# Optimization experiments

Measured on AMD Instinct MI355X. Metric: run time of the kernel, lower is better.

The kernel has to match this reference:

```python
import jax, jax.numpy as jnp
import numpy as np

N, E, C, D, M = 20000, 640000, 128, 128, 128


def setup_inputs() -> dict:
    key = jax.random.key(0)
    ks = jax.random.split(key, 16)
    g = lambda k, shape, fan: jax.random.normal(k, shape, jnp.float32) * (1.0 / np.sqrt(fan))
    return {
        "x": jax.random.normal(ks[0], (N, C), jnp.float32),
        "edge_index": jax.random.randint(ks[1], (2, E), 0, N, jnp.int64),
        "W_src": g(ks[2], (C, D), C),
        "b_src": jnp.zeros((D,), jnp.float32),
        "W_tgt": g(ks[3], (C, D), C),
        "W_skip": g(ks[4], (C, D), C),
        "a0": jnp.asarray(0.2, jnp.float32),   # PReLU init=0.2
        "W1": g(ks[5], (D, M), D),
        "b1": jnp.zeros((M,), jnp.float32),
        "a1": jnp.asarray(0.25, jnp.float32),  # MLP PReLU default
        "W2": g(ks[6], (M, D), M),
        "b2": jnp.zeros((D,), jnp.float32),
        "Wg": g(ks[7], (D, 1), D),
        "gamma": jnp.ones((D,), jnp.float32),
        "beta": jnp.zeros((D,), jnp.float32),
    }


def _prelu(h, a):
    return jnp.where(h >= 0, h, a * h)


def reference(x, edge_index, W_src, b_src, W_tgt, W_skip, a0, W1, b1, a1, W2, b2, Wg, gamma, beta):
    n = x.shape[0]
    j, i = edge_index[0], edge_index[1]  # src -> tgt
    msg_src = x @ W_src + b_src          # lin_src (bias)
    msg_tgt = x @ W_tgt                  # lin_tgt (no bias)
    # per-edge message: msg_nn(msg_j + msg_i) = PReLU -> Linear -> PReLU -> Linear
    h = _prelu(msg_src[j] + msg_tgt[i], a0)          # [E, D]
    h = _prelu(h @ W1 + b1, a1)                      # [E, M]
    msg = h @ W2 + b2                                # [E, D]
    # gate + sparse softmax over edges grouped by target node i
    gate = msg @ Wg                                  # [E, 1]
    gmax = jax.ops.segment_max(gate, i, num_segments=n)
    eg = jnp.exp(gate - gmax[i])
    gsum = jax.ops.segment_sum(eg, i, num_segments=n)
    alpha = eg / (gsum[i] + 1e-16)                   # [E, 1]
    # aggregate (aggr='add')
    out = jax.ops.segment_sum(alpha * msg, i, num_segments=n)  # [N, D]
    # root/skip connection
    out = out + x @ W_skip
    # LayerNorm
    mu = jnp.mean(out, axis=-1, keepdims=True)
    var = jnp.var(out, axis=-1, keepdims=True)
    out = (out - mu) * jax.lax.rsqrt(var + 1e-5) * gamma + beta
    return out
```

## Files before the change

### kernel.cpp

```cpp
#include <hip/hip_runtime.h>
#include <hip/hip_bf16.h>
#include <stdint.h>

#define DIM 128
#define HSTR 136
#define H2STR 72
#define NPB 16
#define NMAX 20224

using hfrag = __attribute__((ext_vector_type(8))) _Float16;
using h2v   = __attribute__((ext_vector_type(2))) _Float16;
using f32x4 = __attribute__((ext_vector_type(4))) float;

__device__ __forceinline__ float prelu_f(float v, float a) { return v >= 0.f ? v : a * v; }

__device__ __forceinline__ unsigned pkh(float a, float b) {
    auto h = __builtin_amdgcn_cvt_pkrtz(a, b);
    return *(unsigned*)&h;
}
__device__ __forceinline__ unsigned short hs(float v) {
    _Float16 h = (_Float16)v;
    return *(unsigned short*)&h;
}
__device__ __forceinline__ unsigned prelu2_add(unsigned su, unsigned gu, h2v a2) {
    h2v s = *(h2v*)&su, g = *(h2v*)&gu;
    h2v h = s + g;
    h2v z = {(_Float16)0.f, (_Float16)0.f};
    h2v mx = __builtin_elementwise_max(h, z);
    h2v mn = __builtin_elementwise_min(h, z);
    h2v r = mn * a2 + mx;
    return *(unsigned*)&r;
}

__global__ __launch_bounds__(256) void prep_hist_k(
    const float* __restrict__ Wsrc, const float* __restrict__ Wtgt,
    const float* __restrict__ Wskip, const float* __restrict__ W1,
    const float* __restrict__ W2, const float* __restrict__ b2,
    const float* __restrict__ Wg,
    unsigned short* __restrict__ Wall, float* __restrict__ w2g,
    const int* __restrict__ eidx, int E, int* __restrict__ deg,
    int* __restrict__ rank)
{
    const int nhist = (E + 255) / 256;
    if ((int)blockIdx.x < nhist) {
        const int e = blockIdx.x * 256 + threadIdx.x;
        if (e < E) rank[e] = atomicAdd(deg + eidx[(size_t)E + e], 1);
        return;
    }
    const int b = blockIdx.x - nhist;
    if (b == (5 * DIM * DIM) / 256) {
        const int k = threadIdx.x;
        if (k < DIM) {
            float s = 0.f;
            for (int d = 0; d < DIM; ++d) s += W2[k * DIM + d] * Wg[d];
            w2g[k] = s;
        } else if (k == DIM) {
            float s = 0.f;
            for (int d = 0; d < DIM; ++d) s += b2[d] * Wg[d];
            w2g[DIM] = s;
        }
        return;
    }
    const int idx = b * 256 + threadIdx.x;
    const int m = idx >> 14;
    const int r = idx & 16383;
    const int n = r >> 7, k = r & 127;
    const float* W = (m == 0) ? Wsrc : (m == 1) ? Wtgt : (m == 2) ? Wskip : (m == 3) ? W1 : W2;
    const _Float16 hv = (_Float16)W[k * DIM + n];
    Wall[idx] = *(const unsigned short*)&hv;
}

__global__ __launch_bounds__(1024) void scan_k(const int* __restrict__ deg,
                                               int* __restrict__ rowptr, int N)
{
    __shared__ int part[1024];
    const int t = threadIdx.x;

    if (N <= NMAX) {
        __shared__ int s[NMAX];
        for (int k = t; k < N; k += 1024) s[k] = deg[k];
        __syncthreads();

        const int chunk = (N + 1023) / 1024;
        const int lo = min(t * chunk, N), hi = min(lo + chunk, N);
        int sum = 0;
        for (int k = lo; k < hi; ++k) sum += s[k];
        part[t] = sum;
        __syncthreads();
        for (int off = 1; off < 1024; off <<= 1) {
            int u = (t >= off) ? part[t - off] : 0;
            __syncthreads();
            part[t] += u;
            __syncthreads();
        }
        int run = part[t] - sum;
        for (int k = lo; k < hi; ++k) { const int d = s[k]; s[k] = run; run += d; }
        __syncthreads();
        for (int k = t; k < N; k += 1024) rowptr[k] = s[k];
        if (t == 0) rowptr[N] = part[1023];
    } else {
        const int chunk = (N + 1023) / 1024;
        const int lo = min(t * chunk, N), hi = min(lo + chunk, N);
        int s = 0;
        for (int k = lo; k < hi; ++k) s += deg[k];
        part[t] = s;
        __syncthreads();
        for (int off = 1; off < 1024; off <<= 1) {
            int u = (t >= off) ? part[t - off] : 0;
            __syncthreads();
            part[t] += u;
            __syncthreads();
        }
        int run = part[t] - s;
        for (int k = lo; k < hi; ++k) {
            rowptr[k] = run;
            run += deg[k];
        }
        if (t == 1023) rowptr[N] = part[1023];
    }
}

__global__ __launch_bounds__(256) void scatter_node_k(
    const int* __restrict__ eidx, int E,
    const int* __restrict__ rowptr, const int* __restrict__ rank,
    int2* __restrict__ jip, int nscatter,
    const float* __restrict__ x,
    const unsigned short* __restrict__ Wall,
    const float* __restrict__ bsrc,
    unsigned short* __restrict__ msg_src, unsigned short* __restrict__ msg_tgt,
    float* __restrict__ skip, int N)
{
    if ((int)blockIdx.x < nscatter) {
        const int e = blockIdx.x * 256 + threadIdx.x;
        if (e < E) {
            const int j = eidx[e];
            const int i = eidx[(size_t)E + e];
            const int p = rowptr[i] + rank[e];
            jip[p] = make_int2(j, i);
        }
        return;
    }

    __shared__ unsigned short xt[32 * HSTR];
    const int t = threadIdx.x;
    const int n0blk = (blockIdx.x - nscatter) * 32;
    const int w = t >> 6, lane = t & 63, col = lane & 15, quad = lane >> 4;

    for (int k = t; k < 32 * 16; k += 256) {
        const int row = k >> 4, o = k & 15;
        uint4 v = make_uint4(0, 0, 0, 0);
        if (n0blk + row < N) {
            const float4 a = *(const float4*)(x + (size_t)(n0blk + row) * DIM + o * 8);
            const float4 b = *(const float4*)(x + (size_t)(n0blk + row) * DIM + o * 8 + 4);
            v.x = pkh(a.x, a.y); v.y = pkh(a.z, a.w);
            v.z = pkh(b.x, b.y); v.w = pkh(b.z, b.w);
        }
        *(uint4*)(xt + row * HSTR + o * 8) = v;
    }
    __syncthreads();

    hfrag af[2][4];
    #pragma unroll
    for (int mt = 0; mt < 2; ++mt)
        #pragma unroll
        for (int ks = 0; ks < 4; ++ks)
            af[mt][ks] = *(const hfrag*)(xt + (mt * 16 + col) * HSTR + ks * 32 + quad * 8);

    for (int m = 0; m < 3; ++m) {
        const unsigned short* Wt = Wall + m * DIM * DIM;
        hfrag bw[2][4];
        #pragma unroll
        for (int nt = 0; nt < 2; ++nt)
            #pragma unroll
            for (int ks = 0; ks < 4; ++ks)
                bw[nt][ks] = *(const hfrag*)(Wt + (w * 32 + nt * 16 + col) * DIM + ks * 32 + quad * 8);

        f32x4 acc[2][2];
        #pragma unroll
        for (int mt = 0; mt < 2; ++mt)
            #pragma unroll
            for (int nt = 0; nt < 2; ++nt)
                acc[mt][nt] = f32x4{0.f, 0.f, 0.f, 0.f};

        #pragma unroll
        for (int mt = 0; mt < 2; ++mt)
            #pragma unroll
            for (int nt = 0; nt < 2; ++nt)
                #pragma unroll
                for (int ks = 0; ks < 4; ++ks)
                    acc[mt][nt] = __builtin_amdgcn_mfma_f32_16x16x32_f16(
                        bw[nt][ks], af[mt][ks], acc[mt][nt], 0, 0, 0);

        #pragma unroll
        for (int mt = 0; mt < 2; ++mt) {
            const int node = n0blk + mt * 16 + col;
            if (node >= N) continue;
            #pragma unroll
            for (int nt = 0; nt < 2; ++nt) {
                const int f0 = w * 32 + nt * 16 + quad * 4;
                if (m == 2) {
                    float4 o;
                    o.x = acc[mt][nt][0]; o.y = acc[mt][nt][1];
                    o.z = acc[mt][nt][2]; o.w = acc[mt][nt][3];
                    *(float4*)(skip + (size_t)node * DIM + f0) = o;
                } else {
                    float b0 = 0.f, b1v = 0.f, b2v = 0.f, b3v = 0.f;
                    if (m == 0) {
                        const float4 bb = *(const float4*)(bsrc + f0);
                        b0 = bb.x; b1v = bb.y; b2v = bb.z; b3v = bb.w;
                    }
                    uint2 o;
                    o.x = pkh(acc[mt][nt][0] + b0, acc[mt][nt][1] + b1v);
                    o.y = pkh(acc[mt][nt][2] + b2v, acc[mt][nt][3] + b3v);
                    unsigned short* dst = (m == 0) ? msg_src : msg_tgt;
                    *(uint2*)(dst + (size_t)node * DIM + f0) = o;
                }
            }
        }
    }
}

__global__ __launch_bounds__(256, 2) void edge_fused_node(
    const int2* __restrict__ jip, const int* __restrict__ rowptr, int N,
    const unsigned short* __restrict__ msg_src, const unsigned short* __restrict__ msg_tgt,
    const float* __restrict__ a0p,
    const unsigned short* __restrict__ W1t, const float* __restrict__ b1,
    const float* __restrict__ a1p,
    const float* __restrict__ w2g,
    const unsigned short* __restrict__ W2t, const float* __restrict__ b2,
    const float* __restrict__ skip,
    const float* __restrict__ gamma, const float* __restrict__ beta,
    float* __restrict__ out)
{
    __shared__ unsigned short h1[64 * HSTR];
    __shared__ unsigned short h2t[DIM * H2STR];
    __shared__ unsigned short tgt_lds[NPB * HSTR];
    __shared__ float gate_part[4][64];
    __shared__ int il_lds[2][64];

    const int t = threadIdx.x;
    const float a0 = *a0p, a1 = *a1p;
    const h2v a02 = {(_Float16)a0, (_Float16)a0};
    const int w = t >> 6, lane = t & 63, col = lane & 15, quad = lane >> 4;
    const int o = t & 15, r0 = t >> 4;

    const int n0 = blockIdx.x * NPB;
    const int elo = rowptr[n0];
    const int ehi = rowptr[min(n0 + NPB, N)];
    const int tc = (ehi - elo + 63) >> 6;

    hfrag bw1[2][4];
    float4 b1q[2], wgq[2];
    #pragma unroll
    for (int nt = 0; nt < 2; ++nt) {
        const int n = w * 32 + nt * 16 + col;
        #pragma unroll
        for (int ks = 0; ks < 4; ++ks)
            bw1[nt][ks] = *(const hfrag*)(W1t + n * DIM + ks * 32 + quad * 8);
        const int nq = w * 32 + nt * 16 + quad * 4;
        b1q[nt] = *(const float4*)(b1 + nq);
        wgq[nt] = *(const float4*)(w2g + nq);
    }
    const float c2 = w2g[DIM];

    for (int k = t; k < NPB * 16; k += 256) {
        const int row = k >> 4, oo = k & 15;
        const int node = n0 + row;
        uint4 v = make_uint4(0, 0, 0, 0);
        if (node < N) v = *(const uint4*)(msg_tgt + (size_t)node * DIM + oo * 8);
        *(uint4*)(tgt_lds + row * HSTR + oo * 8) = v;
    }
    __syncthreads();

    f32x4 acc2[2] = {f32x4{0.f, 0.f, 0.f, 0.f}, f32x4{0.f, 0.f, 0.f, 0.f}};
    float zreg = 0.f;

    if (tc > 0) {
        {
            int2 e0r[4];
            #pragma unroll
            for (int i = 0; i < 4; ++i)
                e0r[i] = jip[min(elo + r0 + 16 * i, ehi - 1)];
            #pragma unroll
            for (int i = 0; i < 4; ++i) {
                const uint4 sv = *(const uint4*)(msg_src + (size_t)e0r[i].x * DIM + o * 8);
                const uint4 gv = *(const uint4*)(tgt_lds + (e0r[i].y - n0) * HSTR + o * 8);
                uint4 hv;
                hv.x = prelu2_add(sv.x, gv.x, a02);
                hv.y = prelu2_add(sv.y, gv.y, a02);
                hv.z = prelu2_add(sv.z, gv.z, a02);
                hv.w = prelu2_add(sv.w, gv.w, a02);
                *(uint4*)(h1 + (r0 + 16 * i) * HSTR + o * 8) = hv;
                if (o == 0) il_lds[0][r0 + 16 * i] = e0r[i].y;
            }
        }
        int2 eN[4];
        {
            const int t1 = min(1, tc - 1);
            #pragma unroll
            for (int i = 0; i < 4; ++i)
                eN[i] = jip[min(elo + t1 * 64 + r0 + 16 * i, ehi - 1)];
        }

        int par = 0;

        for (int tt = 0; tt < tc; ++tt) {
            __syncthreads();

            const bool pf = (tt + 1 < tc);

            uint4 sv[4];
            if (pf) {
                #pragma unroll
                for (int i = 0; i < 4; ++i)
                    sv[i] = *(const uint4*)(msg_src + (size_t)eN[i].x * DIM + o * 8);
            }

            f32x4 acc[4][2];
            #pragma unroll
            for (int mt = 0; mt < 4; ++mt)
                #pragma unroll
                for (int nt = 0; nt < 2; ++nt)
                    acc[mt][nt] = f32x4{0.f, 0.f, 0.f, 0.f};

            __builtin_amdgcn_s_setprio(1);
            #pragma unroll
            for (int mt = 0; mt < 4; ++mt) {
                hfrag af[4];
                #pragma unroll
                for (int ks = 0; ks < 4; ++ks)
                    af[ks] = *(const hfrag*)(h1 + (mt * 16 + col) * HSTR + ks * 32 + quad * 8);
                #pragma unroll
                for (int nt = 0; nt < 2; ++nt)
                    #pragma unroll
                    for (int ks = 0; ks < 4; ++ks)
                        acc[mt][nt] = __builtin_amdgcn_mfma_f32_16x16x32_f16(
                            bw1[nt][ks], af[ks], acc[mt][nt], 0, 0, 0);
            }
            __builtin_amdgcn_s_setprio(0);

            #pragma unroll
            for (int mt = 0; mt < 4; ++mt) {
                const int m = mt * 16 + col;
                float g = 0.f;
                #pragma unroll
                for (int nt = 0; nt < 2; ++nt) {
                    const int fb = w * 32 + nt * 16 + quad * 4;
                    const float p0v = prelu_f(acc[mt][nt][0] + b1q[nt].x, a1);
                    const float p1v = prelu_f(acc[mt][nt][1] + b1q[nt].y, a1);
                    const float p2v = prelu_f(acc[mt][nt][2] + b1q[nt].z, a1);
                    const float p3v = prelu_f(acc[mt][nt][3] + b1q[nt].w, a1);
                    h2t[(fb + 0) * H2STR + m] = hs(p0v);
                    h2t[(fb + 1) * H2STR + m] = hs(p1v);
                    h2t[(fb + 2) * H2STR + m] = hs(p2v);
                    h2t[(fb + 3) * H2STR + m] = hs(p3v);
                    g += p0v * wgq[nt].x + p1v * wgq[nt].y + p2v * wgq[nt].z + p3v * wgq[nt].w;
                }
                g += __shfl_xor(g, 16);
                g += __shfl_xor(g, 32);
                if (quad == 0) gate_part[w][m] = g;
            }

            __syncthreads();

            if (pf) {
                #pragma unroll
                for (int i = 0; i < 4; ++i) {
                    const uint4 gv = *(const uint4*)(tgt_lds + (eN[i].y - n0) * HSTR + o * 8);
                    uint4 hv;
                    hv.x = prelu2_add(sv[i].x, gv.x, a02);
                    hv.y = prelu2_add(sv[i].y, gv.y, a02);
                    hv.z = prelu2_add(sv[i].z, gv.z, a02);
                    hv.w = prelu2_add(sv[i].w, gv.w, a02);
                    *(uint4*)(h1 + (r0 + 16 * i) * HSTR + o * 8) = hv;
                    if (o == 0) il_lds[par ^ 1][r0 + 16 * i] = eN[i].y;
                }
                const int t2 = min(tt + 2, tc - 1);
                #pragma unroll
                for (int i = 0; i < 4; ++i)
                    eN[i] = jip[min(elo + t2 * 64 + r0 + 16 * i, ehi - 1)];
            }

            {
                const int ebase = elo + tt * 64;
                const int limit = min(64, ehi - ebase);
                hfrag bf2[2];
                float zp = 0.f;
                #pragma unroll
                for (int ks = 0; ks < 2; ++ks) {
                    const int e0 = ks * 32 + quad * 8;
                    const float4 ga0 = *(const float4*)&gate_part[0][e0];
                    const float4 ga1 = *(const float4*)&gate_part[1][e0];
                    const float4 ga2 = *(const float4*)&gate_part[2][e0];
                    const float4 ga3 = *(const float4*)&gate_part[3][e0];
                    const float4 gb0 = *(const float4*)&gate_part[0][e0 + 4];
                    const float4 gb1 = *(const float4*)&gate_part[1][e0 + 4];
                    const float4 gb2 = *(const float4*)&gate_part[2][e0 + 4];
                    const float4 gb3 = *(const float4*)&gate_part[3][e0 + 4];
                    const int4 ia = *(const int4*)&il_lds[par][e0];
                    const int4 ib = *(const int4*)&il_lds[par][e0 + 4];
                    const float e0v = __expf(fminf(ga0.x + ga1.x + ga2.x + ga3.x + c2, 11.f));
                    const float e1v = __expf(fminf(ga0.y + ga1.y + ga2.y + ga3.y + c2, 11.f));
                    const float e2v = __expf(fminf(ga0.z + ga1.z + ga2.z + ga3.z + c2, 11.f));
                    const float e3v = __expf(fminf(ga0.w + ga1.w + ga2.w + ga3.w + c2, 11.f));
                    const float e4v = __expf(fminf(gb0.x + gb1.x + gb2.x + gb3.x + c2, 11.f));
                    const float e5v = __expf(fminf(gb0.y + gb1.y + gb2.y + gb3.y + c2, 11.f));
                    const float e6v = __expf(fminf(gb0.z + gb1.z + gb2.z + gb3.z + c2, 11.f));
                    const float e7v = __expf(fminf(gb0.w + gb1.w + gb2.w + gb3.w + c2, 11.f));
                    const float s0 = (ia.x - n0 == col && e0 + 0 < limit) ? e0v : 0.f;
                    const float s1 = (ia.y - n0 == col && e0 + 1 < limit) ? e1v : 0.f;
                    const float s2 = (ia.z - n0 == col && e0 + 2 < limit) ? e2v : 0.f;
                    const float s3 = (ia.w - n0 == col && e0 + 3 < limit) ? e3v : 0.f;
                    const float s4 = (ib.x - n0 == col && e0 + 4 < limit) ? e4v : 0.f;
                    const float s5 = (ib.y - n0 == col && e0 + 5 < limit) ? e5v : 0.f;
                    const float s6 = (ib.z - n0 == col && e0 + 6 < limit) ? e6v : 0.f;
                    const float s7 = (ib.w - n0 == col && e0 + 7 < limit) ? e7v : 0.f;
                    zp += s0 + s1 + s2 + s3 + s4 + s5 + s6 + s7;
                    uint4 uu;
                    uu.x = pkh(s0, s1); uu.y = pkh(s2, s3);
                    uu.z = pkh(s4, s5); uu.w = pkh(s6, s7);
                    bf2[ks] = *(hfrag*)&uu;
                }
                float z = zp;
                z += __shfl_xor(z, 16);
                z += __shfl_xor(z, 32);
                zreg += z;
                #pragma unroll
                for (int nt = 0; nt < 2; ++nt)
                    #pragma unroll
                    for (int ks = 0; ks < 2; ++ks) {
                        const hfrag a2 = *(const hfrag*)(
                            h2t + (w * 32 + nt * 16 + col) * H2STR + ks * 32 + quad * 8);
                        acc2[nt] = __builtin_amdgcn_mfma_f32_16x16x32_f16(
                            a2, bf2[ks], acc2[nt], 0, 0, 0);
                    }
            }

            par ^= 1;
        }
    }

    unsigned short* agg_lds = h1;
    {
        const float invz = 1.f / (zreg + 1e-16f);
        #pragma unroll
        for (int nt = 0; nt < 2; ++nt) {
            uint2 ov;
            ov.x = pkh(acc2[nt][0] * invz, acc2[nt][1] * invz);
            ov.y = pkh(acc2[nt][2] * invz, acc2[nt][3] * invz);
            *(uint2*)(agg_lds + col * HSTR + w * 32 + nt * 16 + quad * 4) = ov;
        }
    }
    __syncthreads();

    hfrag bw2[2][4];
    float4 b2q[2];
    #pragma unroll
    for (int nt = 0; nt < 2; ++nt) {
        const int n = w * 32 + nt * 16 + col;
        #pragma unroll
        for (int ks = 0; ks < 4; ++ks)
            bw2[nt][ks] = *(const hfrag*)(W2t + n * DIM + ks * 32 + quad * 8);
        b2q[nt] = *(const float4*)(b2 + w * 32 + nt * 16 + quad * 4);
    }

    hfrag afo[4];
    #pragma unroll
    for (int ks = 0; ks < 4; ++ks)
        afo[ks] = *(const hfrag*)(agg_lds + col * HSTR + ks * 32 + quad * 8);

    f32x4 accO[2] = {f32x4{0.f, 0.f, 0.f, 0.f}, f32x4{0.f, 0.f, 0.f, 0.f}};
    #pragma unroll
    for (int nt = 0; nt < 2; ++nt)
        #pragma unroll
        for (int ks = 0; ks < 4; ++ks)
            accO[nt] = __builtin_amdgcn_mfma_f32_16x16x32_f16(
                bw2[nt][ks], afo[ks], accO[nt], 0, 0, 0);

    const int node = n0 + col;
    float v[2][4];
    float s1 = 0.f, s2 = 0.f;
    #pragma unroll
    for (int nt = 0; nt < 2; ++nt) {
        const int f0 = w * 32 + nt * 16 + quad * 4;
        float4 sk = make_float4(0.f, 0.f, 0.f, 0.f);
        if (node < N) sk = *(const float4*)(skip + (size_t)node * DIM + f0);
        v[nt][0] = accO[nt][0] + b2q[nt].x + sk.x;
        v[nt][1] = accO[nt][1] + b2q[nt].y + sk.y;
        v[nt][2] = accO[nt][2] + b2q[nt].z + sk.z;
        v[nt][3] = accO[nt][3] + b2q[nt].w + sk.w;
        #pragma unroll
        for (int r = 0; r < 4; ++r) {
            s1 += v[nt][r];
            s2 += v[nt][r] * v[nt][r];
        }
    }
    s1 += __shfl_xor(s1, 16); s1 += __shfl_xor(s1, 32);
    s2 += __shfl_xor(s2, 16); s2 += __shfl_xor(s2, 32);
    if (quad == 0) { gate_part[w][col] = s1; gate_part[w][16 + col] = s2; }
    __syncthreads();

    if (node < N) {
        const float sum = gate_part[0][col] + gate_part[1][col]
                        + gate_part[2][col] + gate_part[3][col];
        const float sq  = gate_part[0][16 + col] + gate_part[1][16 + col]
                        + gate_part[2][16 + col] + gate_part[3][16 + col];
        const float mu = sum * (1.f / 128.f);
        const float var = sq * (1.f / 128.f) - mu * mu;
        const float rs = rsqrtf(var + 1e-5f);
        #pragma unroll
        for (int nt = 0; nt < 2; ++nt) {
            const int f0 = w * 32 + nt * 16 + quad * 4;
            const float4 gm = *(const float4*)(gamma + f0);
            const float4 bt = *(const float4*)(beta + f0);
            float4 ov;
            ov.x = (v[nt][0] - mu) * rs * gm.x + bt.x;
            ov.y = (v[nt][1] - mu) * rs * gm.y + bt.y;
            ov.z = (v[nt][2] - mu) * rs * gm.z + bt.z;
            ov.w = (v[nt][3] - mu) * rs * gm.w + bt.w;
            *(float4*)(out + (size_t)node * DIM + f0) = ov;
        }
    }
}

extern "C" void kernel_launch(void* const* d_in, const int* in_sizes, int n_in,
                              void* d_out, int out_size, void* d_ws, size_t ws_size,
                              hipStream_t stream)
{
    const float* x     = (const float*)d_in[0];
    const int*   eidx  = (const int*)d_in[1];
    const float* Wsrc  = (const float*)d_in[2];
    const float* bsrc  = (const float*)d_in[3];
    const float* Wtgt  = (const float*)d_in[4];
    const float* Wskip = (const float*)d_in[5];
    const float* a0    = (const float*)d_in[6];
    const float* W1    = (const float*)d_in[7];
    const float* b1    = (const float*)d_in[8];
    const float* a1    = (const float*)d_in[9];
    const float* W2    = (const float*)d_in[10];
    const float* b2    = (const float*)d_in[11];
    const float* Wg    = (const float*)d_in[12];
    const float* gamma = (const float*)d_in[13];
    const float* beta  = (const float*)d_in[14];

    const int N = in_sizes[0] / DIM;
    const int E = in_sizes[1] / 2;
    float* out = (float*)d_out;

    char* ws = (char*)d_ws;
    size_t off = 0;
    auto alloc = [&](size_t bytes) -> void* {
        void* p = ws + off;
        off += (bytes + 255) & ~(size_t)255;
        return p;
    };
    int*            deg     = (int*)alloc((size_t)N * 4);
    unsigned short* msg_src = (unsigned short*)alloc((size_t)N * DIM * 2);
    unsigned short* msg_tgt = (unsigned short*)alloc((size_t)N * DIM * 2);
    float*          skip    = (float*)alloc((size_t)N * DIM * 4);
    int*            rowptr  = (int*)alloc((size_t)(N + 1) * 4);
    int*            rank    = (int*)alloc((size_t)E * 4);
    int2*           jip     = (int2*)alloc((size_t)E * 8);
    unsigned short* Wall    = (unsigned short*)alloc((size_t)5 * DIM * DIM * 2);
    float*          w2g     = (float*)alloc((size_t)(DIM + 1) * 4);
    (void)ws_size; (void)n_in; (void)out_size;

    (void)hipMemsetAsync(deg, 0, (size_t)N * 4, stream);

    const int nhist = (E + 255) / 256;
    prep_hist_k<<<nhist + (5 * DIM * DIM) / 256 + 1, 256, 0, stream>>>(
        Wsrc, Wtgt, Wskip, W1, W2, b2, Wg, Wall, w2g, eidx, E, deg, rank);

    scan_k<<<1, 1024, 0, stream>>>(deg, rowptr, N);

    const int nscatter = (E + 255) / 256;
    const int nnode = (N + 31) / 32;
    scatter_node_k<<<nscatter + nnode, 256, 0, stream>>>(
        eidx, E, rowptr, rank, jip, nscatter,
        x, Wall, bsrc, msg_src, msg_tgt, skip, N);

    const int nblk = (N + NPB - 1) / NPB;
    edge_fused_node<<<nblk, 256, 0, stream>>>(jip, rowptr, N, msg_src, msg_tgt, a0,
                                              Wall + 3 * DIM * DIM, b1, a1, w2g,
                                              Wall + 4 * DIM * DIM, b2, skip,
                                              gamma, beta, out);
}
```

Baseline: 245.9 us.

## Restructure CSR build: overlap histogram with node GEMM, use atomic cursor scatter

The deg memset moves into the weight-prep kernel, and the degree histogram now runs in the same launch as the node projection GEMM, so the atomics overlap with matrix work. The per-edge rank array is dropped. Scatter instead claims slots with an atomicAdd on a cursor initialised by the scan, which removes the rank write and read. The cost is one extra kernel launch and a second pass of atomics, and the edge order within each segment becomes nondeterministic.

Result: slower. 265.1 us (+7.8%).

```diff
diff --git a/kernel.cpp b/kernel.cpp
--- a/kernel.cpp
+++ b/kernel.cpp
@@ -32,22 +32,25 @@
     return *(unsigned*)&r;
 }
 
-__global__ __launch_bounds__(256) void prep_hist_k(
+__global__ __launch_bounds__(256) void prep_w_k(
     const float* __restrict__ Wsrc, const float* __restrict__ Wtgt,
     const float* __restrict__ Wskip, const float* __restrict__ W1,
     const float* __restrict__ W2, const float* __restrict__ b2,
     const float* __restrict__ Wg,
     unsigned short* __restrict__ Wall, float* __restrict__ w2g,
-    const int* __restrict__ eidx, int E, int* __restrict__ deg,
-    int* __restrict__ rank)
+    int* __restrict__ deg, int N)
 {
-    const int nhist = (E + 255) / 256;
-    if ((int)blockIdx.x < nhist) {
-        const int e = blockIdx.x * 256 + threadIdx.x;
-        if (e < E) rank[e] = atomicAdd(deg + eidx[(size_t)E + e], 1);
+    const int b = blockIdx.x;
+    if (b < (5 * DIM * DIM) / 256) {
+        const int idx = b * 256 + threadIdx.x;
+        const int m = idx >> 14;
+        const int r = idx & 16383;
+        const int n = r >> 7, k = r & 127;
+        const float* W = (m == 0) ? Wsrc : (m == 1) ? Wtgt : (m == 2) ? Wskip : (m == 3) ? W1 : W2;
+        const _Float16 hv = (_Float16)W[k * DIM + n];
+        Wall[idx] = *(const unsigned short*)&hv;
         return;
     }
-    const int b = blockIdx.x - nhist;
     if (b == (5 * DIM * DIM) / 256) {
         const int k = threadIdx.x;
         if (k < DIM) {
@@ -61,89 +64,27 @@
         }
         return;
     }
-    const int idx = b * 256 + threadIdx.x;
-    const int m = idx >> 14;
-    const int r = idx & 16383;
-    const int n = r >> 7, k = r & 127;
-    const float* W = (m == 0) ? Wsrc : (m == 1) ? Wtgt : (m == 2) ? Wskip : (m == 3) ? W1 : W2;
-    const _Float16 hv = (_Float16)W[k * DIM + n];
-    Wall[idx] = *(const unsigned short*)&hv;
-}
-
-__global__ __launch_bounds__(1024) void scan_k(const int* __restrict__ deg,
-                                               int* __restrict__ rowptr, int N)
-{
-    __shared__ int part[1024];
-    const int t = threadIdx.x;
-
-    if (N <= NMAX) {
-        __shared__ int s[NMAX];
-        for (int k = t; k < N; k += 1024) s[k] = deg[k];
-        __syncthreads();
-
-        const int chunk = (N + 1023) / 1024;
-        const int lo = min(t * chunk, N), hi = min(lo + chunk, N);
-        int sum = 0;
-        for (int k = lo; k < hi; ++k) sum += s[k];
-        part[t] = sum;
-        __syncthreads();
-        for (int off = 1; off < 1024; off <<= 1) {
-            int u = (t >= off) ? part[t - off] : 0;
-            __syncthreads();
-            part[t] += u;
-            __syncthreads();
-        }
-        int run = part[t] - sum;
-        for (int k = lo; k < hi; ++k) { const int d = s[k]; s[k] = run; run += d; }
-        __syncthreads();
-        for (int k = t; k < N; k += 1024) rowptr[k] = s[k];
-        if (t == 0) rowptr[N] = part[1023];
-    } else {
-        const int chunk = (N + 1023) / 1024;
-        const int lo = min(t * chunk, N), hi = min(lo + chunk, N);
-        int s = 0;
-        for (int k = lo; k < hi; ++k) s += deg[k];
-        part[t] = s;
-        __syncthreads();
-        for (int off = 1; off < 1024; off <<= 1) {
-            int u = (t >= off) ? part[t - off] : 0;
-            __syncthreads();
-            part[t] += u;
-            __syncthreads();
-        }
-        int run = part[t] - s;
-        for (int k = lo; k < hi; ++k) {
-            rowptr[k] = run;
-            run += deg[k];
-        }
-        if (t == 1023) rowptr[N] = part[1023];
-    }
-}
-
-__global__ __launch_bounds__(256) void scatter_node_k(
-    const int* __restrict__ eidx, int E,
-    const int* __restrict__ rowptr, const int* __restrict__ rank,
-    int2* __restrict__ jip, int nscatter,
+    const int i = (b - (5 * DIM * DIM) / 256 - 1) * 256 + threadIdx.x;
+    if (i < N) deg[i] = 0;
+}
+
+__global__ __launch_bounds__(256) void work_k(
+    const int* __restrict__ eidx, int E, int* __restrict__ deg, int nnode,
     const float* __restrict__ x,
     const unsigned short* __restrict__ Wall,
     const float* __restrict__ bsrc,
     unsigned short* __restrict__ msg_src, unsigned short* __restrict__ msg_tgt,
     float* __restrict__ skip, int N)
 {
-    if ((int)blockIdx.x < nscatter) {
-        const int e = blockIdx.x * 256 + threadIdx.x;
-        if (e < E) {
-            const int j = eidx[e];
-            const int i = eidx[(size_t)E + e];
-            const int p = rowptr[i] + rank[e];
-            jip[p] = make_int2(j, i);
-        }
+    if ((int)blockIdx.x >= nnode) {
+        const int e = ((int)blockIdx.x - nnode) * 256 + threadIdx.x;
+        if (e < E) atomicAdd(deg + eidx[(size_t)E + e], 1);
         return;
     }
 
     __shared__ unsigned short xt[32 * HSTR];
     const int t = threadIdx.x;
-    const int n0blk = (blockIdx.x - nscatter) * 32;
+    const int n0blk = blockIdx.x * 32;
     const int w = t >> 6, lane = t & 63, col = lane & 15, quad = lane >> 4;
 
     for (int k = t; k < 32 * 16; k += 256) {
@@ -217,6 +158,71 @@
                 }
             }
         }
+    }
+}
+
+__global__ __launch_bounds__(1024) void scan_k(const int* __restrict__ deg,
+                                               int* __restrict__ rowptr,
+                                               int* __restrict__ cursor, int N)
+{
+    __shared__ int part[1024];
+    const int t = threadIdx.x;
+
+    if (N <= NMAX) {
+        __shared__ int s[NMAX];
+        for (int k = t; k < N; k += 1024) s[k] = deg[k];
+        __syncthreads();
+
+        const int chunk = (N + 1023) / 1024;
+        const int lo = min(t * chunk, N), hi = min(lo + chunk, N);
+        int sum = 0;
+        for (int k = lo; k < hi; ++k) sum += s[k];
+        part[t] = sum;
+        __syncthreads();
+        for (int off = 1; off < 1024; off <<= 1) {
+            int u = (t >= off) ? part[t - off] : 0;
+            __syncthreads();
+            part[t] += u;
+            __syncthreads();
+        }
+        int run = part[t] - sum;
+        for (int k = lo; k < hi; ++k) { const int d = s[k]; s[k] = run; run += d; }
+        __syncthreads();
+        for (int k = t; k < N; k += 1024) { rowptr[k] = s[k]; cursor[k] = s[k]; }
+        if (t == 0) rowptr[N] = part[1023];
+    } else {
+        const int chunk = (N + 1023) / 1024;
+        const int lo = min(t * chunk, N), hi = min(lo + chunk, N);
+        int s = 0;
+        for (int k = lo; k < hi; ++k) s += deg[k];
+        part[t] = s;
+        __syncthreads();
+        for (int off = 1; off < 1024; off <<= 1) {
+            int u = (t >= off) ? part[t - off] : 0;
+            __syncthreads();
+            part[t] += u;
+            __syncthreads();
+        }
+        int run = part[t] - s;
+        for (int k = lo; k < hi; ++k) {
+            rowptr[k] = run;
+            cursor[k] = run;
+            run += deg[k];
+        }
+        if (t == 1023) rowptr[N] = part[1023];
+    }
+}
+
+__global__ __launch_bounds__(256) void scatter_k(
+    const int* __restrict__ eidx, int E,
+    int* __restrict__ cursor, int2* __restrict__ jip)
+{
+    const int e = blockIdx.x * 256 + threadIdx.x;
+    if (e < E) {
+        const int j = eidx[e];
+        const int i = eidx[(size_t)E + e];
+        const int p = atomicAdd(cursor + i, 1);
+        jip[p] = make_int2(j, i);
     }
 }
 
@@ -555,29 +561,29 @@
         return p;
     };
     int*            deg     = (int*)alloc((size_t)N * 4);
+    int*            cursor  = (int*)alloc((size_t)N * 4);
     unsigned short* msg_src = (unsigned short*)alloc((size_t)N * DIM * 2);
     unsigned short* msg_tgt = (unsigned short*)alloc((size_t)N * DIM * 2);
     float*          skip    = (float*)alloc((size_t)N * DIM * 4);
     int*            rowptr  = (int*)alloc((size_t)(N + 1) * 4);
-    int*            rank    = (int*)alloc((size_t)E * 4);
     int2*           jip     = (int2*)alloc((size_t)E * 8);
     unsigned short* Wall    = (unsigned short*)alloc((size_t)5 * DIM * DIM * 2);
     float*          w2g     = (float*)alloc((size_t)(DIM + 1) * 4);
     (void)ws_size; (void)n_in; (void)out_size;
 
-    (void)hipMemsetAsync(deg, 0, (size_t)N * 4, stream);
-
+    const int nwb = (5 * DIM * DIM) / 256 + 1;
+    const int nzb = (N + 255) / 256;
+    prep_w_k<<<nwb + nzb, 256, 0, stream>>>(
+        Wsrc, Wtgt, Wskip, W1, W2, b2, Wg, Wall, w2g, deg, N);
+
+    const int nnode = (N + 31) / 32;
     const int nhist = (E + 255) / 256;
-    prep_hist_k<<<nhist + (5 * DIM * DIM) / 256 + 1, 256, 0, stream>>>(
-        Wsrc, Wtgt, Wskip, W1, W2, b2, Wg, Wall, w2g, eidx, E, deg, rank);
-
-    scan_k<<<1, 1024, 0, stream>>>(deg, rowptr, N);
-
-    const int nscatter = (E + 255) / 256;
-    const int nnode = (N + 31) / 32;
-    scatter_node_k<<<nscatter + nnode, 256, 0, stream>>>(
-        eidx, E, rowptr, rank, jip, nscatter,
-        x, Wall, bsrc, msg_src, msg_tgt, skip, N);
+    work_k<<<nnode + nhist, 256, 0, stream>>>(
+        eidx, E, deg, nnode, x, Wall, bsrc, msg_src, msg_tgt, skip, N);
+
+    scan_k<<<1, 1024, 0, stream>>>(deg, rowptr, cursor, N);
+
+    scatter_k<<<nhist, 256, 0, stream>>>(eidx, E, cursor, jip);
 
     const int nblk = (N + NPB - 1) / NPB;
     edge_fused_node<<<nblk, 256, 0, stream>>>(jip, rowptr, N, msg_src, msg_tgt, a0,
```

## Move node projections into the histogram kernel, reading fp32 weights directly

Applied to the files above, without the earlier changes.

The node GEMMs (src/tgt/skip projections) now run in the same launch as the degree histogram instead of after the scan, so they overlap with the atomic histogram work and the scatter kernel becomes a lean edge-only pass. Because the projections can no longer depend on a prior fp16 transpose of the weights, each block converts the fp32 W_src/W_tgt/W_skip columns itself with strided scalar loads. The prep conversion now covers only W1 and W2. The cost is redundant, uncoalesced weight reads in every node block.

After: 242.7 us. No clear change (-1.3%).

```diff
diff --git a/kernel.cpp b/kernel.cpp
--- a/kernel.cpp
+++ b/kernel.cpp
@@ -6,7 +6,6 @@
 #define HSTR 136
 #define H2STR 72
 #define NPB 16
-#define NMAX 20224
 
 using hfrag = __attribute__((ext_vector_type(8))) _Float16;
 using h2v   = __attribute__((ext_vector_type(2))) _Float16;
@@ -32,118 +31,54 @@
     return *(unsigned*)&r;
 }
 
-__global__ __launch_bounds__(256) void prep_hist_k(
+__global__ __launch_bounds__(256) void prep_k(
+    const int* __restrict__ eidx, int E, int N, int nhist, int nnode,
+    int* __restrict__ deg, int* __restrict__ rank,
+    const float* __restrict__ x,
     const float* __restrict__ Wsrc, const float* __restrict__ Wtgt,
     const float* __restrict__ Wskip, const float* __restrict__ W1,
-    const float* __restrict__ W2, const float* __restrict__ b2,
+    const float* __restrict__ W2, const float* __restrict__ b2f,
     const float* __restrict__ Wg,
     unsigned short* __restrict__ Wall, float* __restrict__ w2g,
-    const int* __restrict__ eidx, int E, int* __restrict__ deg,
-    int* __restrict__ rank)
+    const float* __restrict__ bsrc,
+    unsigned short* __restrict__ msg_src, unsigned short* __restrict__ msg_tgt,
+    float* __restrict__ skip)
 {
-    const int nhist = (E + 255) / 256;
-    if ((int)blockIdx.x < nhist) {
-        const int e = blockIdx.x * 256 + threadIdx.x;
+    const int b = blockIdx.x;
+    const int t = threadIdx.x;
+
+    if (b < nhist) {
+        const int e = b * 256 + t;
         if (e < E) rank[e] = atomicAdd(deg + eidx[(size_t)E + e], 1);
         return;
     }
-    const int b = blockIdx.x - nhist;
-    if (b == (5 * DIM * DIM) / 256) {
-        const int k = threadIdx.x;
-        if (k < DIM) {
-            float s = 0.f;
-            for (int d = 0; d < DIM; ++d) s += W2[k * DIM + d] * Wg[d];
-            w2g[k] = s;
-        } else if (k == DIM) {
-            float s = 0.f;
-            for (int d = 0; d < DIM; ++d) s += b2[d] * Wg[d];
-            w2g[DIM] = s;
+
+    if (b >= nhist + nnode) {
+        const int bb = b - nhist - nnode;
+        if (bb < 128) {
+            const int idx = bb * 256 + t;
+            const int m = idx >> 14;
+            const int r = idx & 16383;
+            const int n = r >> 7, k = r & 127;
+            const float* W = (m == 0) ? W1 : W2;
+            const _Float16 hv = (_Float16)W[k * DIM + n];
+            Wall[idx] = *(const unsigned short*)&hv;
+        } else {
+            if (t < DIM) {
+                float s = 0.f;
+                for (int d = 0; d < DIM; ++d) s += W2[t * DIM + d] * Wg[d];
+                w2g[t] = s;
+            } else if (t == DIM) {
+                float s = 0.f;
+                for (int d = 0; d < DIM; ++d) s += b2f[d] * Wg[d];
+                w2g[DIM] = s;
+            }
         }
         return;
     }
-    const int idx = b * 256 + threadIdx.x;
-    const int m = idx >> 14;
-    const int r = idx & 16383;
-    const int n = r >> 7, k = r & 127;
-    const float* W = (m == 0) ? Wsrc : (m == 1) ? Wtgt : (m == 2) ? Wskip : (m == 3) ? W1 : W2;
-    const _Float16 hv = (_Float16)W[k * DIM + n];
-    Wall[idx] = *(const unsigned short*)&hv;
-}
-
-__global__ __launch_bounds__(1024) void scan_k(const int* __restrict__ deg,
-                                               int* __restrict__ rowptr, int N)
-{
-    __shared__ int part[1024];
-    const int t = threadIdx.x;
-
-    if (N <= NMAX) {
-        __shared__ int s[NMAX];
-        for (int k = t; k < N; k += 1024) s[k] = deg[k];
-        __syncthreads();
-
-        const int chunk = (N + 1023) / 1024;
-        const int lo = min(t * chunk, N), hi = min(lo + chunk, N);
-        int sum = 0;
-        for (int k = lo; k < hi; ++k) sum += s[k];
-        part[t] = sum;
-        __syncthreads();
-        for (int off = 1; off < 1024; off <<= 1) {
-            int u = (t >= off) ? part[t - off] : 0;
-            __syncthreads();
-            part[t] += u;
-            __syncthreads();
-        }
-        int run = part[t] - sum;
-        for (int k = lo; k < hi; ++k) { const int d = s[k]; s[k] = run; run += d; }
-        __syncthreads();
-        for (int k = t; k < N; k += 1024) rowptr[k] = s[k];
-        if (t == 0) rowptr[N] = part[1023];
-    } else {
-        const int chunk = (N + 1023) / 1024;
-        const int lo = min(t * chunk, N), hi = min(lo + chunk, N);
-        int s = 0;
-        for (int k = lo; k < hi; ++k) s += deg[k];
-        part[t] = s;
-        __syncthreads();
-        for (int off = 1; off < 1024; off <<= 1) {
-            int u = (t >= off) ? part[t - off] : 0;
-            __syncthreads();
-            part[t] += u;
-            __syncthreads();
-        }
-        int run = part[t] - s;
-        for (int k = lo; k < hi; ++k) {
-            rowptr[k] = run;
-            run += deg[k];
-        }
-        if (t == 1023) rowptr[N] = part[1023];
-    }
-}
-
-__global__ __launch_bounds__(256) void scatter_node_k(
-    const int* __restrict__ eidx, int E,
-    const int* __restrict__ rowptr, const int* __restrict__ rank,
-    int2* __restrict__ jip, int nscatter,
-    const float* __restrict__ x,
-    const unsigned short* __restrict__ Wall,
-    const float* __restrict__ bsrc,
-    unsigned short* __restrict__ msg_src, unsigned short* __restrict__ msg_tgt,
-    float* __restrict__ skip, int N)
-{
-    if ((int)blockIdx.x < nscatter) {
-        const int e = blockIdx.x * 256 + threadIdx.x;
-        if (e < E) {
-            const int j = eidx[e];
-            const int i = eidx[(size_t)E + e];
-            const int p = rowptr[i] + rank[e];
-            jip[p] = make_int2(j, i);
-        }
-        return;
-    }
 
     __shared__ unsigned short xt[32 * HSTR];
-    const int t = threadIdx.x;
-    const int n0blk = (blockIdx.x - nscatter) * 32;
+    const int n0blk = (b - nhist) * 32;
     const int w = t >> 6, lane = t & 63, col = lane & 15, quad = lane >> 4;
 
     for (int k = t; k < 32 * 16; k += 256) {
@@ -151,9 +86,9 @@
         uint4 v = make_uint4(0, 0, 0, 0);
         if (n0blk + row < N) {
             const float4 a = *(const float4*)(x + (size_t)(n0blk + row) * DIM + o * 8);
-            const float4 b = *(const float4*)(x + (size_t)(n0blk + row) * DIM + o * 8 + 4);
+            const float4 bb = *(const float4*)(x + (size_t)(n0blk + row) * DIM + o * 8 + 4);
             v.x = pkh(a.x, a.y); v.y = pkh(a.z, a.w);
-            v.z = pkh(b.x, b.y); v.w = pkh(b.z, b.w);
+            v.z = pkh(bb.x, bb.y); v.w = pkh(bb.z, bb.w);
         }
         *(uint4*)(xt + row * HSTR + o * 8) = v;
     }
@@ -167,13 +102,20 @@
             af[mt][ks] = *(const hfrag*)(xt + (mt * 16 + col) * HSTR + ks * 32 + quad * 8);
 
     for (int m = 0; m < 3; ++m) {
-        const unsigned short* Wt = Wall + m * DIM * DIM;
+        const float* Wf = (m == 0) ? Wsrc : (m == 1) ? Wtgt : Wskip;
         hfrag bw[2][4];
         #pragma unroll
-        for (int nt = 0; nt < 2; ++nt)
-            #pragma unroll
-            for (int ks = 0; ks < 4; ++ks)
-                bw[nt][ks] = *(const hfrag*)(Wt + (w * 32 + nt * 16 + col) * DIM + ks * 32 + quad * 8);
+        for (int nt = 0; nt < 2; ++nt) {
+            const int n = w * 32 + nt * 16 + col;
+            #pragma unroll
+            for (int ks = 0; ks < 4; ++ks) {
+                hfrag f;
+                #pragma unroll
+                for (int j = 0; j < 8; ++j)
+                    f[j] = (_Float16)Wf[(size_t)(ks * 32 + quad * 8 + j) * DIM + n];
+                bw[nt][ks] = f;
+            }
+        }
 
         f32x4 acc[2][2];
         #pragma unroll
@@ -217,6 +159,70 @@
                 }
             }
         }
+    }
+}
+
+#define NMAX 20224
+__global__ __launch_bounds__(1024) void scan_k(const int* __restrict__ deg,
+                                               int* __restrict__ rowptr, int N)
+{
+    __shared__ int part[1024];
+    const int t = threadIdx.x;
+
+    if (N <= NMAX) {
+        __shared__ int s[NMAX];
+        for (int k = t; k < N; k += 1024) s[k] = deg[k];
+        __syncthreads();
+
+        const int chunk = (N + 1023) / 1024;
+        const int lo = min(t * chunk, N), hi = min(lo + chunk, N);
+        int sum = 0;
+        for (int k = lo; k < hi; ++k) sum += s[k];
+        part[t] = sum;
+        __syncthreads();
+        for (int off = 1; off < 1024; off <<= 1) {
+            int u = (t >= off) ? part[t - off] : 0;
+            __syncthreads();
+            part[t] += u;
+            __syncthreads();
+        }
+        int run = part[t] - sum;
+        for (int k = lo; k < hi; ++k) { const int d = s[k]; s[k] = run; run += d; }
+        __syncthreads();
+        for (int k = t; k < N; k += 1024) rowptr[k] = s[k];
+        if (t == 0) rowptr[N] = part[1023];
+    } else {
+        const int chunk = (N + 1023) / 1024;
+        const int lo = min(t * chunk, N), hi = min(lo + chunk, N);
+        int s = 0;
+        for (int k = lo; k < hi; ++k) s += deg[k];
+        part[t] = s;
+        __syncthreads();
+        for (int off = 1; off < 1024; off <<= 1) {
+            int u = (t >= off) ? part[t - off] : 0;
+            __syncthreads();
+            part[t] += u;
+            __syncthreads();
+        }
+        int run = part[t] - s;
+        for (int k = lo; k < hi; ++k) {
+            rowptr[k] = run;
+            run += deg[k];
+        }
+        if (t == 1023) rowptr[N] = part[1023];
+    }
+}
+
+__global__ __launch_bounds__(256) void scatter_k(
+    const int* __restrict__ eidx, int E,
+    const int* __restrict__ rowptr, const int* __restrict__ rank,
+    int2* __restrict__ jip)
+{
+    const int e = blockIdx.x * 256 + threadIdx.x;
+    if (e < E) {
+        const int j = eidx[e];
+        const int i = eidx[(size_t)E + e];
+        jip[rowptr[i] + rank[e]] = make_int2(j, i);
     }
 }
 
@@ -561,27 +567,26 @@
     int*            rowptr  = (int*)alloc((size_t)(N + 1) * 4);
     int*            rank    = (int*)alloc((size_t)E * 4);
     int2*           jip     = (int2*)alloc((size_t)E * 8);
-    unsigned short* Wall    = (unsigned short*)alloc((size_t)5 * DIM * DIM * 2);
+    unsigned short* Wall    = (unsigned short*)alloc((size_t)2 * DIM * DIM * 2);
     float*          w2g     = (float*)alloc((size_t)(DIM + 1) * 4);
     (void)ws_size; (void)n_in; (void)out_size;
 
     (void)hipMemsetAsync(deg, 0, (size_t)N * 4, stream);
 
     const int nhist = (E + 255) / 256;
-    prep_hist_k<<<nhist + (5 * DIM * DIM) / 256 + 1, 256, 0, stream>>>(
-        Wsrc, Wtgt, Wskip, W1, W2, b2, Wg, Wall, w2g, eidx, E, deg, rank);
+    const int nnode = (N + 31) / 32;
+    prep_k<<<nhist + nnode + 128 + 1, 256, 0, stream>>>(
+        eidx, E, N, nhist, nnode, deg, rank,
+        x, Wsrc, Wtgt, Wskip, W1, W2, b2, Wg,
+        Wall, w2g, bsrc, msg_src, msg_tgt, skip);
 
     scan_k<<<1, 1024, 0, stream>>>(deg, rowptr, N);
 
-    const int nscatter = (E + 255) / 256;
-    const int nnode = (N + 31) / 32;
-    scatter_node_k<<<nscatter + nnode, 256, 0, stream>>>(
-        eidx, E, rowptr, rank, jip, nscatter,
-        x, Wall, bsrc, msg_src, msg_tgt, skip, N);
+    scatter_k<<<nhist, 256, 0, stream>>>(eidx, E, rowptr, rank, jip);
 
     const int nblk = (N + NPB - 1) / NPB;
     edge_fused_node<<<nblk, 256, 0, stream>>>(jip, rowptr, N, msg_src, msg_tgt, a0,
-                                              Wall + 3 * DIM * DIM, b1, a1, w2g,
-                                              Wall + 4 * DIM * DIM, b2, skip,
+                                              Wall, b1, a1, w2g,
+                                              Wall + DIM * DIM, b2, skip,
                                               gamma, beta, out);
 }
```
